# Optimization experiments

Hardware: AMD Instinct MI355X
Metric: run time of the kernel (lower is better)

Reference implementation:

```python
import jax, jax.numpy as jnp
import numpy as np

# Standard JPEG luminance quantization table (quality 50)
_QTABLE = np.array([
    [16, 11, 10, 16, 24, 40, 51, 61],
    [12, 12, 14, 19, 26, 58, 60, 55],
    [14, 13, 16, 24, 40, 57, 69, 56],
    [14, 17, 22, 29, 51, 87, 80, 62],
    [18, 22, 37, 56, 68, 109, 103, 77],
    [24, 35, 55, 64, 81, 104, 113, 92],
    [49, 64, 78, 87, 103, 121, 120, 101],
    [72, 92, 95, 98, 112, 100, 103, 99]], dtype=np.float32)

def _dct_mtx(n=8):
    # Orthonormal DCT-II basis matrix: mtx @ block @ mtx.T is the 2-D DCT,
    # so mtx.T @ coeffs @ mtx is the inverse DCT used by this module.
    k = np.arange(n)[:, None]
    j = np.arange(n)[None, :]
    m = np.cos(np.pi * (2 * j + 1) * k / (2 * n)) * np.sqrt(2.0 / n)
    m[0, :] /= np.sqrt(2.0)
    return m.astype(np.float32)

def setup_inputs() -> dict:
    key = jax.random.key(0)
    B, C, H, W = 32, 1, 1024, 1024  # square image required by the reshape chain
    x = jax.random.normal(key, (B, C, H, W), dtype=jnp.float32) * 10.0
    return {
        "x": x,
        "qtable": jnp.asarray(_QTABLE),
        "mtx": jnp.asarray(_dct_mtx(8)),
    }

def reference(x, qtable, mtx):
    B, D1, D2, D3 = x.shape
    # view -> permute -> reshape chain extracting 8x8 blocks (faithful to torch code)
    y = x.reshape(B, D1 * D2 // 8, 8, D3)
    y = jnp.transpose(y, (0, 1, 3, 2))                       # (B, D1*D2/8, D3, 8)
    y = y.reshape(B, D1 * D2 * D3 // 64, 8, 8)
    y = jnp.transpose(y, (0, 1, 3, 2))                       # (B, Nblk, 8, 8)
    y = y * qtable                                           # dequantize
    # mtx.T @ y @ mtx  (batched tiny 8x8 IDCT)
    y = jnp.einsum('ji,bnjk,kl->bnil', mtx, y, mtx)
    # inverse reshape/permute chain back to image layout
    y = jnp.transpose(y, (0, 1, 3, 2))
    y = y.reshape(B, D1 * D2 // 8, D2, 8)
    y = jnp.transpose(y, (0, 1, 3, 2))
    return y.reshape(x.shape) + 128.0
```

## Files before the change

### kernel.cpp

```cpp
#include <hip/hip_runtime.h>


__global__ __launch_bounds__(256, 4) void bidct_kernel(
    const float* __restrict__ x, const float* __restrict__ qt,
    const float* __restrict__ mtx, float* __restrict__ out)
{
    const int n   = blockIdx.x * 256 + threadIdx.x;
    const int img = n >> 14;
    const int m   = n & 16383;
    const int br  = m >> 7;
    const int bc  = m & 127;
    const size_t base = ((size_t)img << 20) + ((size_t)br << 13) + ((size_t)bc << 3);

    const float* __restrict__ px = x + base;

    float T[8][8];
#pragma unroll
    for (int i = 0; i < 8; ++i)
#pragma unroll
        for (int k = 0; k < 8; ++k)
            T[i][k] = 0.0f;

#pragma unroll
    for (int jh = 0; jh < 2; ++jh) {
        float4 xa[4], xb[4];
#pragma unroll
        for (int jj = 0; jj < 4; ++jj) {
            const float* row = px + (size_t)(jh * 4 + jj) * 1024;
            xa[jj] = *reinterpret_cast<const float4*>(row);
            xb[jj] = *reinterpret_cast<const float4*>(row + 4);
        }
#pragma unroll
        for (int jj = 0; jj < 4; ++jj) {
            const int j = jh * 4 + jj;
            float xq[8];
            xq[0] = xa[jj].x * qt[j * 8 + 0];
            xq[1] = xa[jj].y * qt[j * 8 + 1];
            xq[2] = xa[jj].z * qt[j * 8 + 2];
            xq[3] = xa[jj].w * qt[j * 8 + 3];
            xq[4] = xb[jj].x * qt[j * 8 + 4];
            xq[5] = xb[jj].y * qt[j * 8 + 5];
            xq[6] = xb[jj].z * qt[j * 8 + 6];
            xq[7] = xb[jj].w * qt[j * 8 + 7];
#pragma unroll
            for (int i = 0; i < 8; ++i) {
                const float mji = mtx[j * 8 + i];
#pragma unroll
                for (int k = 0; k < 8; ++k)
                    T[i][k] = fmaf(mji, xq[k], T[i][k]);
            }
        }
    }

    float* __restrict__ po = out + base;
#pragma unroll
    for (int i = 0; i < 8; ++i) {
        float o[8] = {128.f, 128.f, 128.f, 128.f, 128.f, 128.f, 128.f, 128.f};
#pragma unroll
        for (int k = 0; k < 8; ++k) {
            const float tk = T[i][k];
#pragma unroll
            for (int l = 0; l < 8; ++l)
                o[l] = fmaf(tk, mtx[k * 8 + l], o[l]);
        }
        float* row = po + (size_t)i * 1024;
        *reinterpret_cast<float4*>(row)     = make_float4(o[0], o[1], o[2], o[3]);
        *reinterpret_cast<float4*>(row + 4) = make_float4(o[4], o[5], o[6], o[7]);
    }
}

extern "C" void kernel_launch(void* const* d_in, const int* in_sizes, int n_in,
                              void* d_out, int out_size, void* d_ws, size_t ws_size,
                              hipStream_t stream) {
    const float* x   = (const float*)d_in[0];
    const float* qt  = (const float*)d_in[1];
    const float* mtx = (const float*)d_in[2];
    float*       out = (float*)d_out;

    const int total_blocks = out_size / 64;
    const int grid         = total_blocks / 256;
    bidct_kernel<<<grid, 256, 0, stream>>>(x, qt, mtx, out);
}
```

Before: 235.9 us.

## Split each 8x8 IDCT block across eight threads, one per output row

Each thread now computes a single output row of a block instead of the whole 8x8 block, with the grid enlarged eight-fold. This cuts per-thread register use (8 accumulators instead of 64) and the amount of serial FMA work per thread, allowing higher occupancy (launch bounds raised). In exchange, every thread reloads the full 8x8 input block, multiplying cache traffic for reads, and redundant dequantization work is done by all eight threads.

```diff
diff --git a/kernel.cpp b/kernel.cpp
--- a/kernel.cpp
+++ b/kernel.cpp
@@ -1,26 +1,26 @@
 #include <hip/hip_runtime.h>
 
 
-__global__ __launch_bounds__(256, 4) void bidct_kernel(
+__global__ __launch_bounds__(256, 8) void bidct_kernel(
     const float* __restrict__ x, const float* __restrict__ qt,
     const float* __restrict__ mtx, float* __restrict__ out)
 {
     const int n   = blockIdx.x * 256 + threadIdx.x;
-    const int img = n >> 14;
-    const int m   = n & 16383;
+    const int b   = n >> 3;
+    const int i   = n & 7;
+    const int img = b >> 14;
+    const int m   = b & 16383;
     const int br  = m >> 7;
     const int bc  = m & 127;
     const size_t base = ((size_t)img << 20) + ((size_t)br << 13) + ((size_t)bc << 3);
 
+    float mcol[8];
+#pragma unroll
+    for (int j = 0; j < 8; ++j) mcol[j] = mtx[j * 8 + i];
+
     const float* __restrict__ px = x + base;
 
-    float T[8][8];
-#pragma unroll
-    for (int i = 0; i < 8; ++i)
-#pragma unroll
-        for (int k = 0; k < 8; ++k)
-            T[i][k] = 0.0f;
-
+    float T[8] = {0.f, 0.f, 0.f, 0.f, 0.f, 0.f, 0.f, 0.f};
 #pragma unroll
     for (int jh = 0; jh < 2; ++jh) {
         float4 xa[4], xb[4];
@@ -33,40 +33,30 @@
 #pragma unroll
         for (int jj = 0; jj < 4; ++jj) {
             const int j = jh * 4 + jj;
-            float xq[8];
-            xq[0] = xa[jj].x * qt[j * 8 + 0];
-            xq[1] = xa[jj].y * qt[j * 8 + 1];
-            xq[2] = xa[jj].z * qt[j * 8 + 2];
-            xq[3] = xa[jj].w * qt[j * 8 + 3];
-            xq[4] = xb[jj].x * qt[j * 8 + 4];
-            xq[5] = xb[jj].y * qt[j * 8 + 5];
-            xq[6] = xb[jj].z * qt[j * 8 + 6];
-            xq[7] = xb[jj].w * qt[j * 8 + 7];
-#pragma unroll
-            for (int i = 0; i < 8; ++i) {
-                const float mji = mtx[j * 8 + i];
-#pragma unroll
-                for (int k = 0; k < 8; ++k)
-                    T[i][k] = fmaf(mji, xq[k], T[i][k]);
-            }
+            const float mj = mcol[j];
+            T[0] = fmaf(mj, xa[jj].x * qt[j * 8 + 0], T[0]);
+            T[1] = fmaf(mj, xa[jj].y * qt[j * 8 + 1], T[1]);
+            T[2] = fmaf(mj, xa[jj].z * qt[j * 8 + 2], T[2]);
+            T[3] = fmaf(mj, xa[jj].w * qt[j * 8 + 3], T[3]);
+            T[4] = fmaf(mj, xb[jj].x * qt[j * 8 + 4], T[4]);
+            T[5] = fmaf(mj, xb[jj].y * qt[j * 8 + 5], T[5]);
+            T[6] = fmaf(mj, xb[jj].z * qt[j * 8 + 6], T[6]);
+            T[7] = fmaf(mj, xb[jj].w * qt[j * 8 + 7], T[7]);
         }
     }
 
-    float* __restrict__ po = out + base;
+    float o[8] = {128.f, 128.f, 128.f, 128.f, 128.f, 128.f, 128.f, 128.f};
 #pragma unroll
-    for (int i = 0; i < 8; ++i) {
-        float o[8] = {128.f, 128.f, 128.f, 128.f, 128.f, 128.f, 128.f, 128.f};
+    for (int k = 0; k < 8; ++k) {
+        const float tk = T[k];
 #pragma unroll
-        for (int k = 0; k < 8; ++k) {
-            const float tk = T[i][k];
-#pragma unroll
-            for (int l = 0; l < 8; ++l)
-                o[l] = fmaf(tk, mtx[k * 8 + l], o[l]);
-        }
-        float* row = po + (size_t)i * 1024;
-        *reinterpret_cast<float4*>(row)     = make_float4(o[0], o[1], o[2], o[3]);
-        *reinterpret_cast<float4*>(row + 4) = make_float4(o[4], o[5], o[6], o[7]);
+        for (int l = 0; l < 8; ++l)
+            o[l] = fmaf(tk, mtx[k * 8 + l], o[l]);
     }
+
+    float* row = out + base + (size_t)i * 1024;
+    *reinterpret_cast<float4*>(row)     = make_float4(o[0], o[1], o[2], o[3]);
+    *reinterpret_cast<float4*>(row + 4) = make_float4(o[4], o[5], o[6], o[7]);
 }
 
 extern "C" void kernel_launch(void* const* d_in, const int* in_sizes, int n_in,
@@ -77,7 +67,6 @@
     const float* mtx = (const float*)d_in[2];
     float*       out = (float*)d_out;
 
-    const int total_blocks = out_size / 64;
-    const int grid         = total_blocks / 256;
+    const int grid = out_size / 2048;
     bidct_kernel<<<grid, 256, 0, stream>>>(x, qt, mtx, out);
 }
```

Measured after the change: 240.7 us. 1.02x slower.
